# Kernel tuning notes

Hardware: AMD Instinct MI355X
Metric: run time of the kernel (lower is better)

Reference implementation:

```python
import jax, jax.numpy as jnp
import numpy as np

B = 8          # batch (number of ragged segments)
N = 4096       # trigram sets per sequence (uniform segments)
K = 3          # trigram token ids per set
V = 100000     # vocab_size
H = 1024       # hidden_size
SEQ = 2048     # sequence_length / seq_len


def setup_inputs() -> dict:
    key = jax.random.key(0)
    k1, k2 = jax.random.split(key)
    trigram_token_ids = jax.random.randint(k1, (B * N, K), 0, V, dtype=jnp.int32)
    # each position covered by exactly 2 trigram sets; per-segment positions start at 0
    pos_one = (jnp.arange(N, dtype=jnp.int32) // 2)  # [N], values 0..SEQ-1
    trigram_set_position_ids = jnp.tile(pos_one, B)  # [B*N]
    starts = jnp.arange(B, dtype=jnp.int32) * N
    trigram_token_ids_offsets = jnp.stack([starts, starts + N], axis=1)  # [B,2]
    std = (2.0 / (5.0 * H)) ** 0.5  # pythia init
    W = jax.random.normal(k2, (V, H), dtype=jnp.float32) * std
    return {
        "trigram_set_position_ids": trigram_set_position_ids,
        "trigram_token_ids": trigram_token_ids,
        "trigram_token_ids_offsets": trigram_token_ids_offsets,
        "seq_len": SEQ,
        "W": W,
    }


def reference(trigram_set_position_ids, trigram_token_ids, trigram_token_ids_offsets, seq_len, W):
    # Uniform ragged segments: reshape flat arrays to [B, n, ...] using offsets count.
    b = trigram_token_ids_offsets.shape[0]
    total, k = trigram_token_ids.shape
    n = total // b
    tok = trigram_token_ids.reshape(b, n, k)          # [B, n, K]
    pos = trigram_set_position_ids.reshape(b, n)      # [B, n]
    # gather + mean-aggregate over the K trigram ids of each set
    emb = W[tok].mean(axis=2)                         # [B, n, H]

    def scatter_one(p, e):
        # index_add scatter of set embeddings onto sequence positions
        s = jax.ops.segment_sum(e, p, num_segments=seq_len)                       # [seq, H]
        c = jax.ops.segment_sum(jnp.ones((n,), e.dtype), p, num_segments=seq_len)  # [seq]
        c = jnp.where(c == 0, jnp.ones((), e.dtype), c)  # counts of 0 -> 1 (normalization guard)
        return s / c[:, None]

    return jax.vmap(scatter_one)(pos, emb)            # [B, seq, H]
```

## Files before the change

kernel.cpp:

```cpp
#include <hip/hip_runtime.h>

#define CAP 8

__global__ void build_map_kernel(const int* __restrict__ pos_ids, int total,
                                 int n_per, int seq,
                                 int* __restrict__ counts,
                                 int* __restrict__ slots) {
    int i = blockIdx.x * blockDim.x + threadIdx.x;
    if (i >= total) return;
    int b = i / n_per;
    int p = pos_ids[i];
    if (p < 0 || p >= seq) return;
    int bp = b * seq + p;
    int c = atomicAdd(&counts[bp], 1);
    if (c < CAP) slots[bp * CAP + c] = i;
}

__global__ void gather_out_kernel(const int* __restrict__ tok,
                                  const float* __restrict__ W,
                                  const int* __restrict__ counts,
                                  const int* __restrict__ slots,
                                  float* __restrict__ out,
                                  int K, int H) {
    int bp = blockIdx.x;
    __shared__ int s_idx[CAP];
    __shared__ int s_cnt;
    if (threadIdx.x == 0) {
        int cnt = counts[bp];
        int ce = cnt < CAP ? cnt : CAP;
        int tmp[CAP];
        for (int j = 0; j < ce; ++j) tmp[j] = slots[bp * CAP + j];
        for (int a = 1; a < ce; ++a) {
            int v = tmp[a];
            int q = a - 1;
            while (q >= 0 && tmp[q] > v) { tmp[q + 1] = tmp[q]; --q; }
            tmp[q + 1] = v;
        }
        for (int j = 0; j < ce; ++j) s_idx[j] = tmp[j];
        s_cnt = cnt;
    }
    __syncthreads();

    int cnt = s_cnt;
    int ce = cnt < CAP ? cnt : CAP;
    int h = threadIdx.x * 4;

    float4 acc = make_float4(0.f, 0.f, 0.f, 0.f);
    for (int j = 0; j < ce; ++j) {
        int base = s_idx[j] * K;
        for (int k = 0; k < K; ++k) {
            int t = tok[base + k];
            const float4 v = *(const float4*)(W + (size_t)t * H + h);
            acc.x += v.x; acc.y += v.y; acc.z += v.z; acc.w += v.w;
        }
    }
    float denom = (float)K * (float)(cnt > 0 ? cnt : 1);
    float scale = 1.0f / denom;
    acc.x *= scale; acc.y *= scale; acc.z *= scale; acc.w *= scale;
    *(float4*)(out + (size_t)bp * H + h) = acc;
}

extern "C" void kernel_launch(void* const* d_in, const int* in_sizes, int n_in,
                              void* d_out, int out_size, void* d_ws, size_t ws_size,
                              hipStream_t stream) {
    const int*   pos_ids = (const int*)d_in[0];
    const int*   tok     = (const int*)d_in[1];
    const float* W       = (const float*)d_in[4];
    float*       out     = (float*)d_out;

    const int B     = in_sizes[2] / 2;
    const int total = in_sizes[0];
    const int n_per = total / B;
    const int K     = in_sizes[1] / total;
    const int H     = 1024;
    const int seq   = out_size / (B * H);

    int* counts = (int*)d_ws;
    int* slots  = counts + (size_t)B * seq;

    hipMemsetAsync(counts, 0, (size_t)B * seq * sizeof(int), stream);

    int bthreads = 256;
    int bblocks  = (total + bthreads - 1) / bthreads;
    build_map_kernel<<<bblocks, bthreads, 0, stream>>>(pos_ids, total, n_per,
                                                       seq, counts, slots);

    gather_out_kernel<<<B * seq, H / 4, 0, stream>>>(tok, W, counts, slots,
                                                     out, K, H);
}
```

Baseline: 83.36 us.

## Store token ids directly in per-position table and specialize six-token gather path

Result: no change. 83.72 us (+0.4%).

```diff
diff --git a/kernel.cpp b/kernel.cpp
--- a/kernel.cpp
+++ b/kernel.cpp
@@ -1,59 +1,76 @@
 #include <hip/hip_runtime.h>
 
 #define CAP 8
+#define MAXK 8
 
-__global__ void build_map_kernel(const int* __restrict__ pos_ids, int total,
-                                 int n_per, int seq,
+__global__ void build_map_kernel(const int* __restrict__ pos_ids,
+                                 const int* __restrict__ tok,
+                                 int total, int n_per, int seq, int K,
                                  int* __restrict__ counts,
-                                 int* __restrict__ slots) {
+                                 int* __restrict__ toktab) {
     int i = blockIdx.x * blockDim.x + threadIdx.x;
     if (i >= total) return;
     int b = i / n_per;
     int p = pos_ids[i];
-    if (p < 0 || p >= seq) return;
+    if ((unsigned)p >= (unsigned)seq) return;
     int bp = b * seq + p;
     int c = atomicAdd(&counts[bp], 1);
-    if (c < CAP) slots[bp * CAP + c] = i;
+    if (c < CAP) {
+        int* dst = toktab + (size_t)bp * (CAP * K) + c * K;
+        for (int k = 0; k < K; ++k) dst[k] = tok[i * K + k];
+    }
 }
 
-__global__ void gather_out_kernel(const int* __restrict__ tok,
-                                  const float* __restrict__ W,
+#define SORT2(a, b) { int _lo = min(a, b); int _hi = max(a, b); a = _lo; b = _hi; }
+
+__global__ void gather_out_kernel(const float* __restrict__ W,
                                   const int* __restrict__ counts,
-                                  const int* __restrict__ slots,
+                                  const int* __restrict__ toktab,
                                   float* __restrict__ out,
                                   int K, int H) {
     int bp = blockIdx.x;
-    __shared__ int s_idx[CAP];
-    __shared__ int s_cnt;
-    if (threadIdx.x == 0) {
-        int cnt = counts[bp];
-        int ce = cnt < CAP ? cnt : CAP;
-        int tmp[CAP];
-        for (int j = 0; j < ce; ++j) tmp[j] = slots[bp * CAP + j];
-        for (int a = 1; a < ce; ++a) {
-            int v = tmp[a];
-            int q = a - 1;
-            while (q >= 0 && tmp[q] > v) { tmp[q + 1] = tmp[q]; --q; }
-            tmp[q + 1] = v;
-        }
-        for (int j = 0; j < ce; ++j) s_idx[j] = tmp[j];
-        s_cnt = cnt;
-    }
-    __syncthreads();
-
-    int cnt = s_cnt;
+    int cnt = counts[bp];
     int ce = cnt < CAP ? cnt : CAP;
+    int ntok = ce * K;
+    const int* tp = toktab + (size_t)bp * (CAP * K);
     int h = threadIdx.x * 4;
 
     float4 acc = make_float4(0.f, 0.f, 0.f, 0.f);
-    for (int j = 0; j < ce; ++j) {
-        int base = s_idx[j] * K;
-        for (int k = 0; k < K; ++k) {
-            int t = tok[base + k];
+
+    if (ntok == 6) {
+        int t0 = tp[0], t1 = tp[1], t2 = tp[2], t3 = tp[3], t4 = tp[4], t5 = tp[5];
+        SORT2(t1, t2) SORT2(t4, t5) SORT2(t0, t2) SORT2(t3, t5)
+        SORT2(t0, t1) SORT2(t3, t4) SORT2(t1, t4) SORT2(t0, t3)
+        SORT2(t2, t5) SORT2(t1, t3) SORT2(t2, t4) SORT2(t2, t3)
+        const float4 v0 = *(const float4*)(W + (size_t)t0 * H + h);
+        const float4 v1 = *(const float4*)(W + (size_t)t1 * H + h);
+        const float4 v2 = *(const float4*)(W + (size_t)t2 * H + h);
+        const float4 v3 = *(const float4*)(W + (size_t)t3 * H + h);
+        const float4 v4 = *(const float4*)(W + (size_t)t4 * H + h);
+        const float4 v5 = *(const float4*)(W + (size_t)t5 * H + h);
+        acc.x = ((v0.x + v1.x) + (v2.x + v3.x)) + (v4.x + v5.x);
+        acc.y = ((v0.y + v1.y) + (v2.y + v3.y)) + (v4.y + v5.y);
+        acc.z = ((v0.z + v1.z) + (v2.z + v3.z)) + (v4.z + v5.z);
+        acc.w = ((v0.w + v1.w) + (v2.w + v3.w)) + (v4.w + v5.w);
+    } else if (ntok > 0) {
+        __shared__ int s_tok[CAP * MAXK];
+        if (threadIdx.x == 0) {
+            for (int j = 0; j < ntok; ++j) s_tok[j] = tp[j];
+            for (int a = 1; a < ntok; ++a) {
+                int v = s_tok[a];
+                int q = a - 1;
+                while (q >= 0 && s_tok[q] > v) { s_tok[q + 1] = s_tok[q]; --q; }
+                s_tok[q + 1] = v;
+            }
+        }
+        __syncthreads();
+        for (int j = 0; j < ntok; ++j) {
+            int t = s_tok[j];
             const float4 v = *(const float4*)(W + (size_t)t * H + h);
             acc.x += v.x; acc.y += v.y; acc.z += v.z; acc.w += v.w;
         }
     }
+
     float denom = (float)K * (float)(cnt > 0 ? cnt : 1);
     float scale = 1.0f / denom;
     acc.x *= scale; acc.y *= scale; acc.z *= scale; acc.w *= scale;
@@ -76,15 +93,16 @@
     const int seq   = out_size / (B * H);
 
     int* counts = (int*)d_ws;
-    int* slots  = counts + (size_t)B * seq;
+    int* toktab = counts + (size_t)B * seq;
 
     hipMemsetAsync(counts, 0, (size_t)B * seq * sizeof(int), stream);
 
     int bthreads = 256;
     int bblocks  = (total + bthreads - 1) / bthreads;
-    build_map_kernel<<<bblocks, bthreads, 0, stream>>>(pos_ids, total, n_per,
-                                                       seq, counts, slots);
+    build_map_kernel<<<bblocks, bthreads, 0, stream>>>(pos_ids, tok, total,
+                                                       n_per, seq, K,
+                                                       counts, toktab);
 
-    gather_out_kernel<<<B * seq, H / 4, 0, stream>>>(tok, W, counts, slots,
+    gather_out_kernel<<<B * seq, H / 4, 0, stream>>>(W, counts, toktab,
                                                      out, K, H);
 }
```
